# Kernel tuning notes

Hardware: AMD Instinct MI355X
Metric: run time of the kernel (lower is better)

Reference implementation:

```python
import jax, jax.numpy as jnp
import numpy as np

N, E = 50000, 800000
NODE_DIM, EDGE_DIM, HID = 128, 32, 128
NEG_SLOPE = 0.2


def _init(key, shape, fan_in):
    # glorot-ish init for weights
    return jax.random.normal(key, shape, dtype=jnp.float32) * (1.0 / np.sqrt(fan_in))


def setup_inputs() -> dict:
    key = jax.random.key(0)
    ks = jax.random.split(key, 20)
    x = jax.random.normal(ks[0], (N, NODE_DIM), dtype=jnp.float32)
    edge_index = jax.random.randint(ks[1], (2, E), 0, N, dtype=jnp.int64)
    edge_attr = jax.random.normal(ks[2], (E, EDGE_DIM), dtype=jnp.float32)
    params = {
        'W_emb': _init(ks[3], (NODE_DIM, HID), NODE_DIM),
        'b_emb': jnp.zeros((HID,), jnp.float32),
        # conv1 (GATv2Conv, heads=1)
        'Wl1': _init(ks[4], (HID, HID), HID), 'bl1': jnp.zeros((HID,), jnp.float32),
        'Wr1': _init(ks[5], (HID, HID), HID),
        'We1': _init(ks[6], (EDGE_DIM, HID), EDGE_DIM),
        'att1': _init(ks[7], (HID,), HID),
        'bo1': jnp.zeros((HID,), jnp.float32),
        # conv2
        'Wl2': _init(ks[8], (HID, HID), HID), 'bl2': jnp.zeros((HID,), jnp.float32),
        'Wr2': _init(ks[9], (HID, HID), HID),
        'We2': _init(ks[10], (EDGE_DIM, HID), EDGE_DIM),
        'att2': _init(ks[11], (HID,), HID),
        'bo2': jnp.zeros((HID,), jnp.float32),
    }
    return {'x': x, 'edge_index': edge_index, 'edge_attr': edge_attr, **params}


def _gatv2(x, src, dst, edge_attr, Wl, bl, Wr, We, att, bo, n_nodes):
    """PyG GATv2Conv (heads=1, add_self_loops=True, fill_value='mean')."""
    xl = x @ Wl + bl          # [N, H] source transform
    xr = x @ Wr               # [N, H] target transform
    # --- add self loops; self-loop edge_attr = mean of incoming edge_attr ---
    ones = jnp.ones((src.shape[0],), x.dtype)
    deg = jax.ops.segment_sum(ones, dst, num_segments=n_nodes)
    loop_attr = jax.ops.segment_sum(edge_attr, dst, num_segments=n_nodes) \
        / jnp.maximum(deg, 1.0)[:, None]
    loops = jnp.arange(n_nodes, dtype=src.dtype)
    src2 = jnp.concatenate([src, loops])
    dst2 = jnp.concatenate([dst, loops])
    ea2 = jnp.concatenate([edge_attr, loop_attr], axis=0)
    # --- per-edge attention (GATv2: leaky_relu AFTER the sum, score via att) ---
    xl_j = xl[src2]                                  # [E', H]
    msg = xl_j + xr[dst2] + ea2 @ We                 # [E', H]
    logits = jax.nn.leaky_relu(msg, NEG_SLOPE) @ att  # [E']
    # --- softmax over incoming edges per target node ---
    m = jax.ops.segment_max(logits, dst2, num_segments=n_nodes)
    ez = jnp.exp(logits - m[dst2])
    denom = jax.ops.segment_sum(ez, dst2, num_segments=n_nodes)
    alpha = ez / denom[dst2]                         # [E']
    # --- scatter-add aggregation ---
    out = jax.ops.segment_sum(alpha[:, None] * xl_j, dst2, num_segments=n_nodes)
    return out + bo


def reference(x, edge_index, edge_attr, W_emb, b_emb,
              Wl1, bl1, Wr1, We1, att1, bo1,
              Wl2, bl2, Wr2, We2, att2, bo2):
    src, dst = edge_index[0], edge_index[1]
    n = x.shape[0]
    h = x @ W_emb + b_emb
    h = jax.nn.silu(_gatv2(h, src, dst, edge_attr, Wl1, bl1, Wr1, We1, att1, bo1, n))
    h = jax.nn.silu(_gatv2(h, src, dst, edge_attr, Wl2, bl2, Wr2, We2, att2, bo2, n))
    return h
```

## Files before the change

kernel.cpp:

```cpp
#include <hip/hip_runtime.h>
#include <hip/hip_bf16.h>
#include <math.h>


#define HIP_N 50000
#define HIP_E 800000
#define HIP_H 128
#define HIP_ED 32
#define NEG_SLOPE 0.2f
#define RESCALE_THR_LOG2 11.5416f
#define LINB ((HIP_N + 31) / 32)
#define SCATB ((HIP_E + 255) / 256)
#define INV_LN2 1.4426950408889634f

typedef __fp16 h2 __attribute__((ext_vector_type(2)));

__device__ __forceinline__ h2 u2h(unsigned int u) {
    union { unsigned int u; h2 h; } c; c.u = u; return c.h;
}
__device__ __forceinline__ unsigned int pkh(float a, float b) {
    union { h2 h; unsigned int u; } c;
    c.h = __builtin_amdgcn_cvt_pkrtz(a, b);
    return c.u;
}

__global__ void k_detect(const int* __restrict__ ei, int* __restrict__ is32) {
    int j = blockIdx.x * blockDim.x + threadIdx.x;
    if (j < 4096) {
        if (ei[2 * j + 1] != 0) atomicOr(is32, 1);
    }
}

__device__ __forceinline__ int fetch_idx(const int* __restrict__ ei, int is32, long long pos) {
    return is32 ? ei[pos] : ei[2 * pos];
}

__global__ void k_hist(const int* __restrict__ ei, const int* __restrict__ flag,
                       int* __restrict__ deg) {
    int is32 = *flag;
    int e = blockIdx.x * blockDim.x + threadIdx.x;
    if (e < HIP_E) {
        int d = fetch_idx(ei, is32, (long long)HIP_E + e);
        atomicAdd(&deg[d], 1);
    }
}

#define SCAN_TILE 1024
#define SCAN_NB ((HIP_N + SCAN_TILE - 1) / SCAN_TILE)

__global__ __launch_bounds__(256) void k_scan1(const int* __restrict__ deg,
                                               int* __restrict__ bsums) {
    __shared__ int ws[4];
    int b = blockIdx.x, t = threadIdx.x;
    int base = b * SCAN_TILE;
    int v = 0;
#pragma unroll
    for (int j = 0; j < 4; ++j) {
        int i = base + t + 256 * j;
        if (i < HIP_N) v += deg[i];
    }
#pragma unroll
    for (int off = 32; off > 0; off >>= 1) v += __shfl_xor(v, off);
    int lane = t & 63, wid = t >> 6;
    if (lane == 0) ws[wid] = v;
    __syncthreads();
    if (t == 0) bsums[b] = ws[0] + ws[1] + ws[2] + ws[3];
}

__global__ __launch_bounds__(64) void k_scan2(const int* __restrict__ bsums,
                                              int* __restrict__ bscan) {
    int t = threadIdx.x;
    int v = (t < SCAN_NB) ? bsums[t] : 0;
    int incl = v;
#pragma unroll
    for (int off = 1; off < 64; off <<= 1) {
        int u = __shfl_up(incl, off);
        if (t >= off) incl += u;
    }
    if (t < SCAN_NB) bscan[t] = incl - v;
}

__global__ __launch_bounds__(1024) void k_scan3(const int* __restrict__ deg,
                                                const int* __restrict__ bscan,
                                                int* __restrict__ offs,
                                                int* __restrict__ cursor) {
    __shared__ int wsum[16];
    int b = blockIdx.x, t = threadIdx.x;
    int i = b * SCAN_TILE + t;
    int lane = t & 63, wid = t >> 6;
    int v = (i < HIP_N) ? deg[i] : 0;
    int incl = v;
#pragma unroll
    for (int off = 1; off < 64; off <<= 1) {
        int u = __shfl_up(incl, off);
        if (lane >= off) incl += u;
    }
    if (lane == 63) wsum[wid] = incl;
    __syncthreads();
    if (wid == 0 && lane < 16) {
        int w = wsum[lane];
#pragma unroll
        for (int off = 1; off < 16; off <<= 1) {
            int u = __shfl_up(w, off);
            if (lane >= off) w += u;
        }
        wsum[lane] = w;
    }
    __syncthreads();
    int baseadd = bscan[b] + (wid > 0 ? wsum[wid - 1] : 0);
    int excl = baseadd + incl - v;
    if (i < HIP_N) {
        offs[i] = excl;
        cursor[i] = excl;
        if (i == HIP_N - 1) offs[HIP_N] = excl + v;
    }
}

__device__ __forceinline__ void lin_body(const float* __restrict__ h,
                                         const float* __restrict__ Wl,
                                         const float* __restrict__ bl,
                                         const float* __restrict__ Wr,
                                         const float* __restrict__ br,
                                         float* __restrict__ xl,
                                         float* __restrict__ xr, int n, int blk) {
    __shared__ float tile[32][128];
    int rb = blk * 32;
    int tid = threadIdx.x;
    for (int j = 0; j < 16; ++j) {
        int idx = j * 256 + tid;
        int r = idx >> 7, c = idx & 127;
        int row = rb + r;
        tile[r][c] = (row < n) ? h[(size_t)row * 128 + c] : 0.f;
    }
    __syncthreads();
    int c = tid & 127, g = tid >> 7;
    float accl[16], accr[16];
#pragma unroll
    for (int r = 0; r < 16; ++r) { accl[r] = 0.f; accr[r] = 0.f; }
    for (int d4 = 0; d4 < 32; ++d4) {
        int d = d4 * 4;
        float wl0 = Wl[(d + 0) * 128 + c];
        float wl1 = Wl[(d + 1) * 128 + c];
        float wl2 = Wl[(d + 2) * 128 + c];
        float wl3 = Wl[(d + 3) * 128 + c];
        float wr0 = Wr[(d + 0) * 128 + c];
        float wr1 = Wr[(d + 1) * 128 + c];
        float wr2 = Wr[(d + 2) * 128 + c];
        float wr3 = Wr[(d + 3) * 128 + c];
#pragma unroll
        for (int r = 0; r < 16; ++r) {
            const float4 hv = *(const float4*)&tile[g * 16 + r][d];
            accl[r] += hv.x * wl0 + hv.y * wl1 + hv.z * wl2 + hv.w * wl3;
            accr[r] += hv.x * wr0 + hv.y * wr1 + hv.z * wr2 + hv.w * wr3;
        }
    }
    float bbl = bl[c], bbr = br[c];
    for (int r = 0; r < 16; ++r) {
        int row = rb + g * 16 + r;
        if (row < n) {
            xl[(size_t)row * 128 + c] = accl[r] + bbl;
            xr[(size_t)row * 128 + c] = accr[r] + bbr;
        }
    }
}

__device__ __forceinline__ void scatter_body(const int* __restrict__ ei, int is32,
                                             int* __restrict__ cursor,
                                             int* __restrict__ e_src,
                                             const float* __restrict__ ea,
                                             unsigned int* __restrict__ ea_h, int e) {
    if (e < HIP_E) {
        int s = fetch_idx(ei, is32, e);
        int d = fetch_idx(ei, is32, (long long)HIP_E + e);
        int pos = atomicAdd(&cursor[d], 1);
        e_src[pos] = s;
        const float4* src4 = (const float4*)(ea + (size_t)e * HIP_ED);
        float4 s0 = src4[0], s1 = src4[1], s2 = src4[2], s3 = src4[3];
        float4 s4 = src4[4], s5 = src4[5], s6 = src4[6], s7 = src4[7];
        uint4* dst = (uint4*)(ea_h + (size_t)pos * 16);
        dst[0] = make_uint4(pkh(s0.x, s0.y), pkh(s0.z, s0.w),
                            pkh(s1.x, s1.y), pkh(s1.z, s1.w));
        dst[1] = make_uint4(pkh(s2.x, s2.y), pkh(s2.z, s2.w),
                            pkh(s3.x, s3.y), pkh(s3.z, s3.w));
        dst[2] = make_uint4(pkh(s4.x, s4.y), pkh(s4.z, s4.w),
                            pkh(s5.x, s5.y), pkh(s5.z, s5.w));
        dst[3] = make_uint4(pkh(s6.x, s6.y), pkh(s6.z, s6.w),
                            pkh(s7.x, s7.y), pkh(s7.z, s7.w));
    }
}

__global__ __launch_bounds__(256) void k_fat1(
    const float* __restrict__ x, const float* __restrict__ Wl,
    const float* __restrict__ bl, const float* __restrict__ Wr,
    const float* __restrict__ br, float* __restrict__ xl, float* __restrict__ xr,
    const int* __restrict__ ei, const int* __restrict__ flag,
    int* __restrict__ cursor, int* __restrict__ e_src,
    const float* __restrict__ ea, unsigned int* __restrict__ ea_h) {
    if (blockIdx.x < LINB) {
        lin_body(x, Wl, bl, Wr, br, xl, xr, HIP_N, blockIdx.x);
    } else {
        int e = (blockIdx.x - LINB) * 256 + threadIdx.x;
        scatter_body(ei, *flag, cursor, e_src, ea, ea_h, e);
    }
}

__global__ __launch_bounds__(256) void k_lin(const float* __restrict__ h,
                                             const float* __restrict__ Wl,
                                             const float* __restrict__ bl,
                                             const float* __restrict__ Wr,
                                             const float* __restrict__ br,
                                             float* __restrict__ xl,
                                             float* __restrict__ xr, int n) {
    lin_body(h, Wl, bl, Wr, br, xl, xr, n, blockIdx.x);
}

__global__ __launch_bounds__(128) void k_compose(
    const float* __restrict__ Wemb, const float* __restrict__ bemb,
    const float* __restrict__ Wl, const float* __restrict__ bl,
    const float* __restrict__ Wr,
    float* __restrict__ Wlf, float* __restrict__ blf,
    float* __restrict__ Wrf, float* __restrict__ brf,
    float* __restrict__ zerob) {
    int b = blockIdx.x, c = threadIdx.x;
    if (b < 128) {
        float acc = 0.f;
        for (int k = 0; k < 128; ++k) acc += Wemb[b * 128 + k] * Wl[k * 128 + c];
        Wlf[b * 128 + c] = acc;
    } else if (b < 256) {
        int r = b - 128;
        float acc = 0.f;
        for (int k = 0; k < 128; ++k) acc += Wemb[r * 128 + k] * Wr[k * 128 + c];
        Wrf[r * 128 + c] = acc;
    } else if (b == 256) {
        float acc = bl[c];
        for (int k = 0; k < 128; ++k) acc += bemb[k] * Wl[k * 128 + c];
        blf[c] = acc;
    } else {
        float acc = 0.f;
        for (int k = 0; k < 128; ++k) acc += bemb[k] * Wr[k * 128 + c];
        brf[c] = acc;
        zerob[c] = 0.f;
    }
}

__global__ __launch_bounds__(256) void k_packwe(const float* __restrict__ We1,
                                                const float* __restrict__ We2,
                                                unsigned int* __restrict__ P1,
                                                unsigned int* __restrict__ P2) {
    int idx = blockIdx.x * 256 + threadIdx.x;
    if (idx < 4096) {
        const float* We = (idx < 2048) ? We1 : We2;
        unsigned int* P = (idx < 2048) ? P1 : P2;
        int r = idx & 2047;
        int d2 = r >> 7, rem = r & 127;
        int j = rem >> 6, t = rem & 63;
        int col = 2 * t + j;
        P[r] = pkh(We[(2 * d2) * 128 + col], We[(2 * d2 + 1) * 128 + col]);
    }
}

__global__ __launch_bounds__(128) void k_node_fused(
    const int* __restrict__ offs, const int* __restrict__ e_src,
    const unsigned int* __restrict__ ea_h,
    const unsigned int* __restrict__ Wepk, const float* __restrict__ att,
    const float* __restrict__ xl, const float* __restrict__ xr,
    const float* __restrict__ bo, float* __restrict__ hout) {
    int i = __builtin_amdgcn_readfirstlane(blockIdx.x * 2 + (threadIdx.x >> 6));
    int t = threadIdx.x & 63;
    if (i >= HIP_N) return;

    h2 wx00 = u2h(Wepk[ 0*128 + t]),      wy00 = u2h(Wepk[ 0*128 + 64 + t]);
    h2 wx01 = u2h(Wepk[ 1*128 + t]),      wy01 = u2h(Wepk[ 1*128 + 64 + t]);
    h2 wx02 = u2h(Wepk[ 2*128 + t]),      wy02 = u2h(Wepk[ 2*128 + 64 + t]);
    h2 wx03 = u2h(Wepk[ 3*128 + t]),      wy03 = u2h(Wepk[ 3*128 + 64 + t]);
    h2 wx04 = u2h(Wepk[ 4*128 + t]),      wy04 = u2h(Wepk[ 4*128 + 64 + t]);
    h2 wx05 = u2h(Wepk[ 5*128 + t]),      wy05 = u2h(Wepk[ 5*128 + 64 + t]);
    h2 wx06 = u2h(Wepk[ 6*128 + t]),      wy06 = u2h(Wepk[ 6*128 + 64 + t]);
    h2 wx07 = u2h(Wepk[ 7*128 + t]),      wy07 = u2h(Wepk[ 7*128 + 64 + t]);
    h2 wx08 = u2h(Wepk[ 8*128 + t]),      wy08 = u2h(Wepk[ 8*128 + 64 + t]);
    h2 wx09 = u2h(Wepk[ 9*128 + t]),      wy09 = u2h(Wepk[ 9*128 + 64 + t]);
    h2 wx10 = u2h(Wepk[10*128 + t]),      wy10 = u2h(Wepk[10*128 + 64 + t]);
    h2 wx11 = u2h(Wepk[11*128 + t]),      wy11 = u2h(Wepk[11*128 + 64 + t]);
    h2 wx12 = u2h(Wepk[12*128 + t]),      wy12 = u2h(Wepk[12*128 + 64 + t]);
    h2 wx13 = u2h(Wepk[13*128 + t]),      wy13 = u2h(Wepk[13*128 + 64 + t]);
    h2 wx14 = u2h(Wepk[14*128 + t]),      wy14 = u2h(Wepk[14*128 + 64 + t]);
    h2 wx15 = u2h(Wepk[15*128 + t]),      wy15 = u2h(Wepk[15*128 + 64 + t]);

    float2 attv = ((const float2*)att)[t];
    attv.x *= INV_LN2; attv.y *= INV_LN2;
    float2 bov  = ((const float2*)bo)[t];
    float2 xri  = ((const float2*)(xr + (size_t)i * HIP_H))[t];
    float2 xli  = ((const float2*)(xl + (size_t)i * HIP_H))[t];

    float m = -1e30f;
    float denom = 0.f;
    float accx = 0.f, accy = 0.f;
    float epsx = 0.f, epsy = 0.f;

    int o0 = offs[i], o1 = offs[i + 1];
    int cnt = o1 - o0;
    int pairs = cnt >> 1;
    const float2* xl2 = (const float2*)xl;

#define DOTP(EX, EY, U, K)                                            \
    EX = __builtin_amdgcn_fdot2(u2h(U), wx##K, EX, false);            \
    EY = __builtin_amdgcn_fdot2(u2h(U), wy##K, EY, false);

#define EPROJ(EX, EY, P)                                              \
    {                                                                 \
        uint4 q0 = ((const uint4*)(P))[0];                            \
        uint4 q1 = ((const uint4*)(P))[1];                            \
        uint4 q2 = ((const uint4*)(P))[2];                            \
        uint4 q3 = ((const uint4*)(P))[3];                            \
        DOTP(EX, EY, q0.x, 00) DOTP(EX, EY, q0.y, 01)                 \
        DOTP(EX, EY, q0.z, 02) DOTP(EX, EY, q0.w, 03)                 \
        DOTP(EX, EY, q1.x, 04) DOTP(EX, EY, q1.y, 05)                 \
        DOTP(EX, EY, q1.z, 06) DOTP(EX, EY, q1.w, 07)                 \
        DOTP(EX, EY, q2.x, 08) DOTP(EX, EY, q2.y, 09)                 \
        DOTP(EX, EY, q2.z, 10) DOTP(EX, EY, q2.w, 11)                 \
        DOTP(EX, EY, q3.x, 12) DOTP(EX, EY, q3.y, 13)                 \
        DOTP(EX, EY, q3.z, 14) DOTP(EX, EY, q3.w, 15)                 \
    }

    float2 xA = make_float2(0.f, 0.f), xB = make_float2(0.f, 0.f);
    if (pairs > 0) {
        int s0 = e_src[o0];
        int s1 = e_src[o0 + 1];
        xA = xl2[(size_t)s0 * 64 + t];
        xB = xl2[(size_t)s1 * 64 + t];
    }

    for (int pp = 0; pp < pairs; ++pp) {
        int e = o0 + 2 * pp;
        float2 x0 = xA, x1 = xB;
        if (pp + 1 < pairs) {
            int s0 = e_src[e + 2];
            int s1 = e_src[e + 3];
            xA = xl2[(size_t)s0 * 64 + t];
            xB = xl2[(size_t)s1 * 64 + t];
        }
        const unsigned int* er = ea_h + (size_t)e * 16;
        float ex0 = 0.f, ey0 = 0.f, ex1 = 0.f, ey1 = 0.f;
        EPROJ(ex0, ey0, er)
        EPROJ(ex1, ey1, er + 16)
        epsx += ex0 + ex1; epsy += ey0 + ey1;
        float vx0 = x0.x + xri.x + ex0, vy0 = x0.y + xri.y + ey0;
        float vx1 = x1.x + xri.x + ex1, vy1 = x1.y + xri.y + ey1;
        vx0 = fmaxf(vx0, NEG_SLOPE * vx0);
        vy0 = fmaxf(vy0, NEG_SLOPE * vy0);
        vx1 = fmaxf(vx1, NEG_SLOPE * vx1);
        vy1 = fmaxf(vy1, NEG_SLOPE * vy1);
        float p0 = vx0 * attv.x + vy0 * attv.y;
        float p1 = vx1 * attv.x + vy1 * attv.y;
#pragma unroll
        for (int off = 32; off > 0; off >>= 1) {
            p0 += __shfl_xor(p0, off);
            p1 += __shfl_xor(p1, off);
        }
        float pm = fmaxf(p0, p1);
        if (pm > m + RESCALE_THR_LOG2) {
            float sc = exp2f(m - pm);
            accx *= sc; accy *= sc; denom *= sc;
            m = pm;
        }
        float wA = exp2f(p0 - m);
        float wB = exp2f(p1 - m);
        accx += wA * x0.x + wB * x1.x;
        accy += wA * x0.y + wB * x1.y;
        denom += wA + wB;
    }

    if (cnt & 1) {
        int e = o1 - 1;
        int s = e_src[e];
        float2 x0 = xl2[(size_t)s * 64 + t];
        const unsigned int* er = ea_h + (size_t)e * 16;
        float ex = 0.f, ey = 0.f;
        EPROJ(ex, ey, er)
        epsx += ex; epsy += ey;
        float vx = x0.x + xri.x + ex;
        float vy = x0.y + xri.y + ey;
        vx = fmaxf(vx, NEG_SLOPE * vx);
        vy = fmaxf(vy, NEG_SLOPE * vy);
        float p = vx * attv.x + vy * attv.y;
#pragma unroll
        for (int off = 32; off > 0; off >>= 1) p += __shfl_xor(p, off);
        if (p > m + RESCALE_THR_LOG2) {
            float sc = exp2f(m - p);
            accx *= sc; accy *= sc; denom *= sc;
            m = p;
        }
        float w = exp2f(p - m);
        accx += w * x0.x;
        accy += w * x0.y;
        denom += w;
    }
#undef EPROJ
#undef DOTP

    float invdeg = 1.f / fmaxf((float)cnt, 1.f);
    float sx = xli.x + xri.x + epsx * invdeg;
    float sy = xli.y + xri.y + epsy * invdeg;
    sx = fmaxf(sx, NEG_SLOPE * sx);
    sy = fmaxf(sy, NEG_SLOPE * sy);
    float ps = sx * attv.x + sy * attv.y;
#pragma unroll
    for (int off = 32; off > 0; off >>= 1) ps += __shfl_xor(ps, off);

    float mm = fmaxf(m, ps);
    float wf = exp2f(m - mm);
    float ws = exp2f(ps - mm);
    denom = denom * wf + ws;
    accx = accx * wf + ws * xli.x;
    accy = accy * wf + ws * xli.y;

    float ox = accx / denom + bov.x;
    float oy = accy / denom + bov.y;
    float2 o;
    o.x = ox / (1.f + __expf(-ox));
    o.y = oy / (1.f + __expf(-oy));
    ((float2*)(hout + (size_t)i * HIP_H))[t] = o;
}

extern "C" void kernel_launch(void* const* d_in, const int* in_sizes, int n_in,
                              void* d_out, int out_size, void* d_ws, size_t ws_size,
                              hipStream_t stream) {
    const float* x      = (const float*)d_in[0];
    const int*   ei     = (const int*)d_in[1];
    const float* ea     = (const float*)d_in[2];
    const float* W_emb  = (const float*)d_in[3];
    const float* b_emb  = (const float*)d_in[4];
    const float* Wl1    = (const float*)d_in[5];
    const float* bl1    = (const float*)d_in[6];
    const float* Wr1    = (const float*)d_in[7];
    const float* We1    = (const float*)d_in[8];
    const float* att1   = (const float*)d_in[9];
    const float* bo1    = (const float*)d_in[10];
    const float* Wl2    = (const float*)d_in[11];
    const float* bl2    = (const float*)d_in[12];
    const float* Wr2    = (const float*)d_in[13];
    const float* We2    = (const float*)d_in[14];
    const float* att2   = (const float*)d_in[15];
    const float* bo2    = (const float*)d_in[16];
    float* out = (float*)d_out;

    char* p = (char*)d_ws;
    auto carve = [&](size_t bytes) {
        void* q = (void*)p;
        p += (bytes + 255) / 256 * 256;
        return q;
    };
    float* h        = (float*)carve((size_t)HIP_N * 128 * 4);
    float* xl       = (float*)carve((size_t)HIP_N * 128 * 4);
    float* xr       = (float*)carve((size_t)HIP_N * 128 * 4);
    unsigned int* ea_h = (unsigned int*)carve((size_t)HIP_E * 16 * 4);
    int*   deg      = (int*)carve((size_t)HIP_N * 4);
    int*   offs     = (int*)carve((size_t)(HIP_N + 1) * 4);
    int*   cursor   = (int*)carve((size_t)HIP_N * 4);
    int*   e_src    = (int*)carve((size_t)HIP_E * 4);
    int*   flag     = (int*)carve(256);
    int*   bsums    = (int*)carve((size_t)SCAN_NB * 4);
    int*   bscan    = (int*)carve((size_t)SCAN_NB * 4);
    float* Wl1f     = (float*)carve(128 * 128 * 4);
    float* Wr1f     = (float*)carve(128 * 128 * 4);
    float* bl1f     = (float*)carve(128 * 4);
    float* br1f     = (float*)carve(128 * 4);
    float* zerob    = (float*)carve(128 * 4);
    unsigned int* Wepk1 = (unsigned int*)carve(2048 * 4);
    unsigned int* Wepk2 = (unsigned int*)carve(2048 * 4);

    hipMemsetAsync(deg, 0, (size_t)HIP_N * 4, stream);
    hipMemsetAsync(flag, 0, 4, stream);

    k_detect<<<16, 256, 0, stream>>>(ei, flag);
    k_hist<<<(HIP_E + 255) / 256, 256, 0, stream>>>(ei, flag, deg);
    k_scan1<<<SCAN_NB, 256, 0, stream>>>(deg, bsums);
    k_scan2<<<1, 64, 0, stream>>>(bsums, bscan);
    k_scan3<<<SCAN_NB, 1024, 0, stream>>>(deg, bscan, offs, cursor);
    k_compose<<<258, 128, 0, stream>>>(W_emb, b_emb, Wl1, bl1, Wr1,
                                       Wl1f, bl1f, Wr1f, br1f, zerob);
    k_packwe<<<16, 256, 0, stream>>>(We1, We2, Wepk1, Wepk2);

    k_fat1<<<LINB + SCATB, 256, 0, stream>>>(x, Wl1f, bl1f, Wr1f, br1f, xl, xr,
                                             ei, flag, cursor, e_src, ea, ea_h);

    int fuse_grid = (HIP_N + 1) / 2;
    k_node_fused<<<fuse_grid, 128, 0, stream>>>(offs, e_src, ea_h, Wepk1, att1,
                                                xl, xr, bo1, h);
    k_lin<<<(HIP_N + 31) / 32, 256, 0, stream>>>(h, Wl2, bl2, Wr2, zerob, xl, xr, HIP_N);
    k_node_fused<<<fuse_grid, 128, 0, stream>>>(offs, e_src, ea_h, Wepk2, att2,
                                                xl, xr, bo2, out);
}
```

Baseline: 507.5 us.

## Store xl/xr node projections in fp16 and launch one node per 64-thread block

The linear kernels now pack their xl and xr outputs to fp16 pairs, using a lane shuffle so each even column writes a packed word. This halves the storage and the gather traffic for the per-edge source feature loads in the fused attention kernel, which unpacks them to float. The attention kernel also switches from two nodes per 128-thread block to one node per 64-thread block. The cost is fp16 rounding of the projected features, which may affect accuracy.

```diff
diff --git a/kernel.cpp b/kernel.cpp
--- a/kernel.cpp
+++ b/kernel.cpp
@@ -22,6 +22,10 @@
     union { h2 h; unsigned int u; } c;
     c.h = __builtin_amdgcn_cvt_pkrtz(a, b);
     return c.u;
+}
+__device__ __forceinline__ float2 h2f(unsigned int u) {
+    h2 h = u2h(u);
+    return make_float2((float)h.x, (float)h.y);
 }
 
 __global__ void k_detect(const int* __restrict__ ei, int* __restrict__ is32) {
@@ -121,8 +125,9 @@
                                          const float* __restrict__ bl,
                                          const float* __restrict__ Wr,
                                          const float* __restrict__ br,
-                                         float* __restrict__ xl,
-                                         float* __restrict__ xr, int n, int blk) {
+                                         unsigned int* __restrict__ xlh,
+                                         unsigned int* __restrict__ xrh,
+                                         int n, int blk) {
     __shared__ float tile[32][128];
     int rb = blk * 32;
     int tid = threadIdx.x;
@@ -155,11 +160,17 @@
         }
     }
     float bbl = bl[c], bbr = br[c];
+    bool evenc = !(c & 1);
+#pragma unroll
     for (int r = 0; r < 16; ++r) {
         int row = rb + g * 16 + r;
-        if (row < n) {
-            xl[(size_t)row * 128 + c] = accl[r] + bbl;
-            xr[(size_t)row * 128 + c] = accr[r] + bbr;
+        float vl = accl[r] + bbl;
+        float vr = accr[r] + bbr;
+        float vl1 = __shfl_down(vl, 1);
+        float vr1 = __shfl_down(vr, 1);
+        if (evenc && row < n) {
+            xlh[(size_t)row * 64 + (c >> 1)] = pkh(vl, vl1);
+            xrh[(size_t)row * 64 + (c >> 1)] = pkh(vr, vr1);
         }
     }
 }
@@ -192,12 +203,13 @@
 __global__ __launch_bounds__(256) void k_fat1(
     const float* __restrict__ x, const float* __restrict__ Wl,
     const float* __restrict__ bl, const float* __restrict__ Wr,
-    const float* __restrict__ br, float* __restrict__ xl, float* __restrict__ xr,
+    const float* __restrict__ br,
+    unsigned int* __restrict__ xlh, unsigned int* __restrict__ xrh,
     const int* __restrict__ ei, const int* __restrict__ flag,
     int* __restrict__ cursor, int* __restrict__ e_src,
     const float* __restrict__ ea, unsigned int* __restrict__ ea_h) {
     if (blockIdx.x < LINB) {
-        lin_body(x, Wl, bl, Wr, br, xl, xr, HIP_N, blockIdx.x);
+        lin_body(x, Wl, bl, Wr, br, xlh, xrh, HIP_N, blockIdx.x);
     } else {
         int e = (blockIdx.x - LINB) * 256 + threadIdx.x;
         scatter_body(ei, *flag, cursor, e_src, ea, ea_h, e);
@@ -209,9 +221,9 @@
                                              const float* __restrict__ bl,
                                              const float* __restrict__ Wr,
                                              const float* __restrict__ br,
-                                             float* __restrict__ xl,
-                                             float* __restrict__ xr, int n) {
-    lin_body(h, Wl, bl, Wr, br, xl, xr, n, blockIdx.x);
+                                             unsigned int* __restrict__ xlh,
+                                             unsigned int* __restrict__ xrh, int n) {
+    lin_body(h, Wl, bl, Wr, br, xlh, xrh, n, blockIdx.x);
 }
 
 __global__ __launch_bounds__(128) void k_compose(
@@ -259,15 +271,14 @@
     }
 }
 
-__global__ __launch_bounds__(128) void k_node_fused(
+__global__ __launch_bounds__(64) void k_node_fused(
     const int* __restrict__ offs, const int* __restrict__ e_src,
     const unsigned int* __restrict__ ea_h,
     const unsigned int* __restrict__ Wepk, const float* __restrict__ att,
-    const float* __restrict__ xl, const float* __restrict__ xr,
+    const unsigned int* __restrict__ xlh, const unsigned int* __restrict__ xrh,
     const float* __restrict__ bo, float* __restrict__ hout) {
-    int i = __builtin_amdgcn_readfirstlane(blockIdx.x * 2 + (threadIdx.x >> 6));
-    int t = threadIdx.x & 63;
-    if (i >= HIP_N) return;
+    int i = blockIdx.x;
+    int t = threadIdx.x;
 
     h2 wx00 = u2h(Wepk[ 0*128 + t]),      wy00 = u2h(Wepk[ 0*128 + 64 + t]);
     h2 wx01 = u2h(Wepk[ 1*128 + t]),      wy01 = u2h(Wepk[ 1*128 + 64 + t]);
@@ -289,8 +300,8 @@
     float2 attv = ((const float2*)att)[t];
     attv.x *= INV_LN2; attv.y *= INV_LN2;
     float2 bov  = ((const float2*)bo)[t];
-    float2 xri  = ((const float2*)(xr + (size_t)i * HIP_H))[t];
-    float2 xli  = ((const float2*)(xl + (size_t)i * HIP_H))[t];
+    float2 xri  = h2f(xrh[(size_t)i * 64 + t]);
+    float2 xli  = h2f(xlh[(size_t)i * 64 + t]);
 
     float m = -1e30f;
     float denom = 0.f;
@@ -300,7 +311,6 @@
     int o0 = offs[i], o1 = offs[i + 1];
     int cnt = o1 - o0;
     int pairs = cnt >> 1;
-    const float2* xl2 = (const float2*)xl;
 
 #define DOTP(EX, EY, U, K)                                            \
     EX = __builtin_amdgcn_fdot2(u2h(U), wx##K, EX, false);            \
@@ -322,22 +332,22 @@
         DOTP(EX, EY, q3.z, 14) DOTP(EX, EY, q3.w, 15)                 \
     }
 
-    float2 xA = make_float2(0.f, 0.f), xB = make_float2(0.f, 0.f);
+    unsigned int uA = 0, uB = 0;
     if (pairs > 0) {
         int s0 = e_src[o0];
         int s1 = e_src[o0 + 1];
-        xA = xl2[(size_t)s0 * 64 + t];
-        xB = xl2[(size_t)s1 * 64 + t];
+        uA = xlh[(size_t)s0 * 64 + t];
+        uB = xlh[(size_t)s1 * 64 + t];
     }
 
     for (int pp = 0; pp < pairs; ++pp) {
         int e = o0 + 2 * pp;
-        float2 x0 = xA, x1 = xB;
+        float2 x0 = h2f(uA), x1 = h2f(uB);
         if (pp + 1 < pairs) {
             int s0 = e_src[e + 2];
             int s1 = e_src[e + 3];
-            xA = xl2[(size_t)s0 * 64 + t];
-            xB = xl2[(size_t)s1 * 64 + t];
+            uA = xlh[(size_t)s0 * 64 + t];
+            uB = xlh[(size_t)s1 * 64 + t];
         }
         const unsigned int* er = ea_h + (size_t)e * 16;
         float ex0 = 0.f, ey0 = 0.f, ex1 = 0.f, ey1 = 0.f;
@@ -373,7 +383,7 @@
     if (cnt & 1) {
         int e = o1 - 1;
         int s = e_src[e];
-        float2 x0 = xl2[(size_t)s * 64 + t];
+        float2 x0 = h2f(xlh[(size_t)s * 64 + t]);
         const unsigned int* er = ea_h + (size_t)e * 16;
         float ex = 0.f, ey = 0.f;
         EPROJ(ex, ey, er)
@@ -451,8 +461,8 @@
         return q;
     };
     float* h        = (float*)carve((size_t)HIP_N * 128 * 4);
-    float* xl       = (float*)carve((size_t)HIP_N * 128 * 4);
-    float* xr       = (float*)carve((size_t)HIP_N * 128 * 4);
+    unsigned int* xlh = (unsigned int*)carve((size_t)HIP_N * 64 * 4);
+    unsigned int* xrh = (unsigned int*)carve((size_t)HIP_N * 64 * 4);
     unsigned int* ea_h = (unsigned int*)carve((size_t)HIP_E * 16 * 4);
     int*   deg      = (int*)carve((size_t)HIP_N * 4);
     int*   offs     = (int*)carve((size_t)(HIP_N + 1) * 4);
@@ -481,13 +491,12 @@
                                        Wl1f, bl1f, Wr1f, br1f, zerob);
     k_packwe<<<16, 256, 0, stream>>>(We1, We2, Wepk1, Wepk2);
 
-    k_fat1<<<LINB + SCATB, 256, 0, stream>>>(x, Wl1f, bl1f, Wr1f, br1f, xl, xr,
+    k_fat1<<<LINB + SCATB, 256, 0, stream>>>(x, Wl1f, bl1f, Wr1f, br1f, xlh, xrh,
                                              ei, flag, cursor, e_src, ea, ea_h);
 
-    int fuse_grid = (HIP_N + 1) / 2;
-    k_node_fused<<<fuse_grid, 128, 0, stream>>>(offs, e_src, ea_h, Wepk1, att1,
-                                                xl, xr, bo1, h);
-    k_lin<<<(HIP_N + 31) / 32, 256, 0, stream>>>(h, Wl2, bl2, Wr2, zerob, xl, xr, HIP_N);
-    k_node_fused<<<fuse_grid, 128, 0, stream>>>(offs, e_src, ea_h, Wepk2, att2,
-                                                xl, xr, bo2, out);
-}
+    k_node_fused<<<HIP_N, 64, 0, stream>>>(offs, e_src, ea_h, Wepk1, att1,
+                                           xlh, xrh, bo1, h);
+    k_lin<<<(HIP_N + 31) / 32, 256, 0, stream>>>(h, Wl2, bl2, Wr2, zerob, xlh, xrh, HIP_N);
+    k_node_fused<<<HIP_N, 64, 0, stream>>>(offs, e_src, ea_h, Wepk2, att2,
+                                           xlh, xrh, bo2, out);
+}
```

Result: faster. 496.5 us (-2.2%).
